# Kernel optimization log

Hardware: AMD Instinct MI355X
Metric: run time of the kernel (lower is better)

Reference implementation:

```python
import math
import jax, jax.numpy as jnp
import numpy as np

B, L, C, H = 8, 1024, 1024, 16
D = C // H  # head_dim = 64
MAX_SCALE_MUL = math.log(100.0)


def setup_inputs() -> dict:
    key = jax.random.key(0)
    ks = jax.random.split(key, 8)
    x = jax.random.normal(ks[0], (B, L, C), dtype=jnp.float32)
    # rotary frequencies: angle(l, j) = l * theta^(-2j/D), stored as (cos, sin)
    theta = 10000.0
    inv_freq = theta ** (-jnp.arange(0, D, 2, dtype=jnp.float32) / D)  # [D/2]
    ang = jnp.arange(L, dtype=jnp.float32)[:, None] * inv_freq[None, :]  # [L, D/2]
    freqs_cis = jnp.stack([jnp.cos(ang), jnp.sin(ang)], axis=-1)  # [L, D/2, 2]
    attn_bias = jnp.zeros((1, 1, L, L), dtype=jnp.float32)
    W_qkv = jax.random.normal(ks[1], (3 * C, C), dtype=jnp.float32) * (1.0 / math.sqrt(C))
    q_bias = jnp.zeros((C,), dtype=jnp.float32)
    v_bias = jnp.zeros((C,), dtype=jnp.float32)
    scale_mul_log = jnp.full((1, H, 1, 1), math.log(4.0), dtype=jnp.float32)
    W_proj = jax.random.normal(ks[2], (C, C), dtype=jnp.float32) * (1.0 / math.sqrt(C))
    b_proj = jnp.zeros((C,), dtype=jnp.float32)
    return {"x": x, "freqs_cis": freqs_cis, "attn_bias": attn_bias,
            "W_qkv": W_qkv, "q_bias": q_bias, "v_bias": v_bias,
            "scale_mul_log": scale_mul_log, "W_proj": W_proj, "b_proj": b_proj}


def _l2norm(t):
    # F.normalize(t, dim=-1): t / max(||t||_2, eps)
    n = jnp.sqrt(jnp.sum(t * t, axis=-1, keepdims=True))
    return t / jnp.maximum(n, 1e-12)


def _rope(t, fr):
    # t: [B,H,L,D]; fr: [L,D/2,2] (cos,sin). Complex mul on adjacent pairs.
    b, h, l, d = t.shape
    t2 = t.reshape(b, h, l, d // 2, 2)
    c = fr[None, None, :, :, 0]
    s = fr[None, None, :, :, 1]
    re = t2[..., 0] * c - t2[..., 1] * s
    im = t2[..., 0] * s + t2[..., 1] * c
    return jnp.stack([re, im], axis=-1).reshape(b, h, l, d)


def reference(x, freqs_cis, attn_bias, W_qkv, q_bias, v_bias, scale_mul_log, W_proj, b_proj):
    b, l, c = x.shape
    bias = jnp.concatenate([q_bias, jnp.zeros_like(q_bias), v_bias])  # [3C]
    qkv = (x @ W_qkv.T + bias).reshape(b, l, 3, H, D)
    # permute(2,0,3,1,4) -> q,k,v each [B,H,L,D]
    q = jnp.transpose(qkv[:, :, 0], (0, 2, 1, 3))
    k = jnp.transpose(qkv[:, :, 1], (0, 2, 1, 3))
    v = jnp.transpose(qkv[:, :, 2], (0, 2, 1, 3))
    # attn_l2_norm path: learned per-head scale, softmax scale = 1
    scale_mul = jnp.exp(jnp.minimum(scale_mul_log, MAX_SCALE_MUL))  # [1,H,1,1]
    q = _l2norm(q) * scale_mul
    k = _l2norm(k)
    q = _rope(q, freqs_cis)
    k = _rope(k, freqs_cis)
    scores = jnp.einsum('bhqd,bhkd->bhqk', q, k) * 1.0 + attn_bias
    attn = jax.nn.softmax(scores, axis=-1)
    out = jnp.einsum('bhqk,bhkd->bhqd', attn, v)
    out = jnp.transpose(out, (0, 2, 1, 3)).reshape(b, l, c)
    return out @ W_proj.T + b_proj
```

## Files before the change

kernel.cpp:

```cpp
#include <hip/hip_runtime.h>
#include <math.h>

#define PB 8
#define PL 1024
#define PC 1024
#define PH 16
#define PD 64
#define MAX_SCALE_MUL 4.605170185988092f
#define LOG2E 1.4426950408889634f

typedef __attribute__((ext_vector_type(8))) short s16x8;
typedef __attribute__((ext_vector_type(4))) float f32x4;

#define MFMA16(a, b, c) __builtin_amdgcn_mfma_f32_16x16x32_bf16(a, b, c, 0, 0, 0)

#if __has_builtin(__builtin_amdgcn_exp2f)
#define EXP2(x) __builtin_amdgcn_exp2f(x)
#else
#define EXP2(x) exp2f(x)
#endif

__device__ __forceinline__ unsigned short f2bf(float f) {
    unsigned u = __float_as_uint(f);
    unsigned r = (u + 0x7fffu + ((u >> 16) & 1u)) >> 16;
    return (unsigned short)r;
}

__device__ __forceinline__ unsigned pk2bf(float a, float b) {
#if __has_builtin(__builtin_amdgcn_cvt_pk_bf16_f32)
    typedef __attribute__((ext_vector_type(2))) __bf16 bf16x2_t;
    bf16x2_t r = __builtin_amdgcn_cvt_pk_bf16_f32(a, b);
    return __builtin_bit_cast(unsigned, r);
#else
    return (unsigned)f2bf(a) | ((unsigned)f2bf(b) << 16);
#endif
}

__device__ __forceinline__ void gl2lds16(const void* g, void* l) {
    __builtin_amdgcn_global_load_lds(
        (const __attribute__((address_space(1))) unsigned int*)g,
        (__attribute__((address_space(3))) unsigned int*)l, 16, 0, 0);
}

__global__ __launch_bounds__(256) void cast3f_kernel(
    const float* __restrict__ a, const float* __restrict__ b,
    const float* __restrict__ c, const float* __restrict__ bias,
    unsigned short* __restrict__ oa, unsigned short* __restrict__ ob,
    unsigned short* __restrict__ oc, int* __restrict__ flag)
{
    int blk = blockIdx.x;
    if (blk >= 12288) {
        int idx = (blk - 12288) * 256 + threadIdx.x;
        const float4* b4 = (const float4*)bias;
        bool nz = false;
#pragma unroll
        for (int i = 0; i < 4; i++) {
            float4 v = b4[idx * 4 + i];
            nz |= (v.x != 0.f) | (v.y != 0.f) | (v.z != 0.f) | (v.w != 0.f);
        }
        if (nz) atomicOr(flag, 1);
        return;
    }
    const float* src; unsigned short* dst; int base;
    if (blk < 8192)       { src = a; dst = oa; base = blk; }
    else if (blk < 11264) { src = b; dst = ob; base = blk - 8192; }
    else                  { src = c; dst = oc; base = blk - 11264; }
    int i = base * 256 + threadIdx.x;
    float4 v = ((const float4*)src)[i];
    ((uint2*)dst)[i] = make_uint2(pk2bf(v.x, v.y), pk2bf(v.z, v.w));
}

template<int VMODE>
__global__ __launch_bounds__(256) void gemm_qkv_lean(
    const unsigned short* __restrict__ Xh,
    const unsigned short* __restrict__ Wh,
    const float* __restrict__ qb, const float* __restrict__ vb,
    const float* __restrict__ freqs,
    unsigned short* __restrict__ Qh, unsigned short* __restrict__ Kh,
    unsigned short* __restrict__ Vt)
{
    __shared__ unsigned short As[128 * 64];
    __shared__ unsigned short Bs[128 * 64];
    const int tid  = threadIdx.x;
    const int wave = tid >> 6, lane = tid & 63;
    const int wm = wave & 1, wn = wave >> 1;
    const int quad = lane >> 4, rr = lane & 15;
    const int m0 = blockIdx.x * 128;
    const int n0 = (blockIdx.y + (VMODE ? 16 : 0)) * 128;

    f32x4 acc[4][4];
#pragma unroll
    for (int i = 0; i < 4; i++)
#pragma unroll
        for (int j = 0; j < 4; j++) acc[i][j] = (f32x4){0.f, 0.f, 0.f, 0.f};

    const int r8 = lane >> 3;
    const int c8 = lane & 7;
    const int g  = c8 ^ r8;
    const unsigned short* gA = Xh + (size_t)(m0 + wave * 32 + r8) * 1024 + g * 8;
    const unsigned short* gB = Wh + (size_t)(n0 + wave * 32 + r8) * 1024 + g * 8;
    unsigned short* lA = &As[(wave * 32) * 64];
    unsigned short* lB = &Bs[(wave * 32) * 64];

    const int swz8 = rr & 7;

    for (int k0 = 0; k0 < 16; k0++) {
#pragma unroll
        for (int t = 0; t < 4; t++) {
            gl2lds16(gA + (size_t)t * 8192, &lA[(t * 8) * 64]);
            gl2lds16(gB + (size_t)t * 8192, &lB[(t * 8) * 64]);
        }
        gA += 64; gB += 64;
        __syncthreads();

#pragma unroll
        for (int kk = 0; kk < 2; kk++) {
            const int coff = ((kk * 4 + quad) ^ swz8) * 8;
            s16x8 wf[4], xf[4];
#pragma unroll
            for (int i = 0; i < 4; i++)
                wf[i] = *(const s16x8*)&Bs[(wn * 64 + i * 16 + rr) * 64 + coff];
#pragma unroll
            for (int j = 0; j < 4; j++)
                xf[j] = *(const s16x8*)&As[(wm * 64 + j * 16 + rr) * 64 + coff];
            if constexpr (VMODE == 0) {
#pragma unroll
                for (int i = 0; i < 4; i++)
#pragma unroll
                    for (int j = 0; j < 4; j++)
                        acc[i][j] = MFMA16(wf[i], xf[j], acc[i][j]);
            } else {
#pragma unroll
                for (int i = 0; i < 4; i++)
#pragma unroll
                    for (int j = 0; j < 4; j++)
                        acc[i][j] = MFMA16(xf[j], wf[i], acc[i][j]);
            }
        }
        __syncthreads();
    }

    const int b   = m0 >> 10;
    const int h   = ((n0 & 1023) + wn * 64) >> 6;
    const int lb0 = (m0 & 1023) + wm * 64;

    if constexpr (VMODE) {
        unsigned short* basep = Vt + (size_t)(b * PH + h) * PD * PL;
#pragma unroll
        for (int i = 0; i < 4; i++) {
            const int d = i * 16 + rr;
            const float bv = vb[h * 64 + d];
#pragma unroll
            for (int j = 0; j < 4; j++) {
                const int l0 = lb0 + j * 16 + quad * 4;
                uint2 pk = make_uint2(pk2bf(acc[i][j][0] + bv, acc[i][j][1] + bv),
                                      pk2bf(acc[i][j][2] + bv, acc[i][j][3] + bv));
                *(uint2*)(basep + (size_t)d * PL + l0) = pk;
            }
        }
    } else {
        const int which = n0 >> 10;
        if (which == 0) {
            unsigned short* basep = Qh + (size_t)(b * PH + h) * PL * PD;
#pragma unroll
            for (int i = 0; i < 4; i++) {
                const int d0 = i * 16 + quad * 4;
                const float4 b4 = *(const float4*)(qb + h * 64 + d0);
#pragma unroll
                for (int j = 0; j < 4; j++) {
                    const int l = lb0 + j * 16 + rr;
                    uint2 pk = make_uint2(
                        pk2bf(acc[i][j][0] + b4.x, acc[i][j][1] + b4.y),
                        pk2bf(acc[i][j][2] + b4.z, acc[i][j][3] + b4.w));
                    *(uint2*)(basep + (size_t)l * PD + d0) = pk;
                }
            }
        } else {
            unsigned short* basep = Kh + (size_t)(b * PH + h) * PL * PD;
            const float2* fr2 = (const float2*)freqs;
#pragma unroll
            for (int j = 0; j < 4; j++) {
                float ss = 0.f;
#pragma unroll
                for (int i = 0; i < 4; i++)
                    ss = fmaf(acc[i][j][0], acc[i][j][0],
                         fmaf(acc[i][j][1], acc[i][j][1],
                         fmaf(acc[i][j][2], acc[i][j][2],
                         fmaf(acc[i][j][3], acc[i][j][3], ss))));
                ss += __shfl_xor(ss, 16);
                ss += __shfl_xor(ss, 32);
                const float scale = 1.0f / fmaxf(sqrtf(ss), 1e-12f);
                const int l = lb0 + j * 16 + rr;
#pragma unroll
                for (int i = 0; i < 4; i++) {
                    const int d0 = i * 16 + quad * 4;
                    const float2 cs0 = fr2[(size_t)l * 32 + (d0 >> 1)];
                    const float2 cs1 = fr2[(size_t)l * 32 + (d0 >> 1) + 1];
                    const float a0 = acc[i][j][0] * scale, a1 = acc[i][j][1] * scale;
                    const float a2 = acc[i][j][2] * scale, a3 = acc[i][j][3] * scale;
                    uint2 pk = make_uint2(
                        pk2bf(a0 * cs0.x - a1 * cs0.y, fmaf(a0, cs0.y, a1 * cs0.x)),
                        pk2bf(a2 * cs1.x - a3 * cs1.y, fmaf(a2, cs1.y, a3 * cs1.x)));
                    *(uint2*)(basep + (size_t)l * PD + d0) = pk;
                }
            }
        }
    }
}

__global__ __launch_bounds__(256) void attn_mfma(
    const unsigned short* __restrict__ Qh, const unsigned short* __restrict__ Kh,
    const unsigned short* __restrict__ Vt, const float* __restrict__ bias,
    const float* __restrict__ sml, const int* __restrict__ biasflag,
    const float* __restrict__ freqs, unsigned short* __restrict__ O)
{
    __shared__ unsigned short Ks[2][64 * 64];
    __shared__ unsigned short Vs[2][64 * 64];
    __shared__ unsigned int   Ps[4][16 * 32];

    const int tid  = threadIdx.x;
    const int wave = tid >> 6, lane = tid & 63;
    const int quad = lane >> 4, rr = lane & 15;
    const int bh = blockIdx.x, q0 = blockIdx.y * 128;
    const int b = bh >> 4, h = bh & 15;
    const int hasbias = *biasflag;

    const float M = __expf(fminf(sml[h], MAX_SCALE_MUL)) * LOG2E;
    const f32x4 negM = (f32x4){-M, -M, -M, -M};

    const int sr = wave * 16 + (lane >> 3);
    const int sc = lane & 7;
    const int sg = sc ^ (sr & 7);
    const int swz8 = rr & 7;
    const int psw  = (rr & 7) << 2;

    const size_t kvbase = (size_t)bh * PL * PD;
    const float2* fr2 = (const float2*)freqs;

    auto stage = [&](int buf, int kb) {
        gl2lds16(Kh + kvbase + (size_t)(kb * 64 + sr) * PD + sg * 8,
                 &Ks[buf][(wave * 16) * 64]);
        gl2lds16(Kh + kvbase + (size_t)(kb * 64 + sr + 8) * PD + sg * 8,
                 &Ks[buf][(wave * 16 + 8) * 64]);
        gl2lds16(Vt + kvbase + (size_t)sr * PL + kb * 64 + sg * 8,
                 &Vs[buf][(wave * 16) * 64]);
        gl2lds16(Vt + kvbase + (size_t)(sr + 8) * PL + kb * 64 + sg * 8,
                 &Vs[buf][(wave * 16 + 8) * 64]);
    };

    stage(0, 0);

    s16x8 qB[2][2];
#pragma unroll
    for (int g = 0; g < 2; g++) {
        const int ql = q0 + g * 64 + wave * 16 + rr;
        const size_t qoff = ((size_t)bh * PL + ql) * PD;
        uint4 r0 = *(const uint4*)(Qh + qoff + quad * 8);
        uint4 r1 = *(const uint4*)(Qh + qoff + 32 + quad * 8);
        unsigned uu[8] = {r0.x, r0.y, r0.z, r0.w, r1.x, r1.y, r1.z, r1.w};
        float lo[8], hi[8];
        float ss = 0.f;
#pragma unroll
        for (int m = 0; m < 8; m++) {
            lo[m] = __uint_as_float(uu[m] << 16);
            hi[m] = __uint_as_float(uu[m] & 0xffff0000u);
            ss = fmaf(lo[m], lo[m], fmaf(hi[m], hi[m], ss));
        }
        ss += __shfl_xor(ss, 16);
        ss += __shfl_xor(ss, 32);
        const float scale = M / fmaxf(sqrtf(ss), 1e-12f);
        unsigned outw[8];
#pragma unroll
        for (int m = 0; m < 8; m++) {
            const int idx = (m >> 2) * 16 + quad * 4 + (m & 3);
            float2 cs = fr2[(size_t)ql * 32 + idx];
            float av = lo[m] * scale, bv = hi[m] * scale;
            float re = av * cs.x - bv * cs.y;
            float im = fmaf(av, cs.y, bv * cs.x);
            outw[m] = pk2bf(re, im);
        }
        uint4 w0 = make_uint4(outw[0], outw[1], outw[2], outw[3]);
        uint4 w1 = make_uint4(outw[4], outw[5], outw[6], outw[7]);
        qB[g][0] = __builtin_bit_cast(s16x8, w0);
        qB[g][1] = __builtin_bit_cast(s16x8, w1);
    }

    f32x4 accO[2][4];
#pragma unroll
    for (int g = 0; g < 2; g++)
#pragma unroll
        for (int jd = 0; jd < 4; jd++) accO[g][jd] = (f32x4){0.f, 0.f, 0.f, 0.f};
    float lsum[2] = {0.f, 0.f};

    __syncthreads();

    int cur = 0;
    for (int kb = 0; kb < 16; kb++) {
        if (kb < 15) stage(cur ^ 1, kb + 1);

        s16x8 kA[4][2];
#pragma unroll
        for (int s = 0; s < 4; s++) {
            kA[s][0] = *(const s16x8*)&Ks[cur][(s * 16 + rr) * 64 + ((0 + quad) ^ swz8) * 8];
            kA[s][1] = *(const s16x8*)&Ks[cur][(s * 16 + rr) * 64 + ((4 + quad) ^ swz8) * 8];
        }
        f32x4 sc4[2][4];
        __builtin_amdgcn_s_setprio(1);
#pragma unroll
        for (int g = 0; g < 2; g++)
#pragma unroll
            for (int s = 0; s < 4; s++) {
                f32x4 z = MFMA16(kA[s][0], qB[g][0], negM);
                z = MFMA16(kA[s][1], qB[g][1], z);
                sc4[g][s] = z;
            }
        __builtin_amdgcn_s_setprio(0);

        if (hasbias) {
#pragma unroll
            for (int g = 0; g < 2; g++) {
                const float* brow = bias + (size_t)(q0 + g * 64 + wave * 16 + rr) * PL + kb * 64;
#pragma unroll
                for (int s = 0; s < 4; s++) {
                    float4 bv = *(const float4*)(brow + s * 16 + quad * 4);
                    sc4[g][s][0] = fmaf(bv.x, LOG2E, sc4[g][s][0]);
                    sc4[g][s][1] = fmaf(bv.y, LOG2E, sc4[g][s][1]);
                    sc4[g][s][2] = fmaf(bv.z, LOG2E, sc4[g][s][2]);
                    sc4[g][s][3] = fmaf(bv.w, LOG2E, sc4[g][s][3]);
                }
            }
        }

#pragma unroll
        for (int g = 0; g < 2; g++) {
#pragma unroll
            for (int s = 0; s < 4; s++) {
                sc4[g][s][0] = EXP2(sc4[g][s][0]);
                sc4[g][s][1] = EXP2(sc4[g][s][1]);
                sc4[g][s][2] = EXP2(sc4[g][s][2]);
                sc4[g][s][3] = EXP2(sc4[g][s][3]);
            }
            f32x4 ls4 = (sc4[g][0] + sc4[g][1]) + (sc4[g][2] + sc4[g][3]);
            lsum[g] += (ls4[0] + ls4[1]) + (ls4[2] + ls4[3]);
        }

        s16x8 vA[4][2];
#pragma unroll
        for (int s = 0; s < 4; s++) {
            vA[s][0] = *(const s16x8*)&Vs[cur][(s * 16 + rr) * 64 + ((0 + quad) ^ swz8) * 8];
            vA[s][1] = *(const s16x8*)&Vs[cur][(s * 16 + rr) * 64 + ((4 + quad) ^ swz8) * 8];
        }
#pragma unroll
        for (int g = 0; g < 2; g++) {
#pragma unroll
            for (int s = 0; s < 4; s++) {
                *(uint2*)&Ps[wave][rr * 32 + ((s * 8 + quad * 2) ^ psw)] =
                    make_uint2(pk2bf(sc4[g][s][0], sc4[g][s][1]),
                               pk2bf(sc4[g][s][2], sc4[g][s][3]));
            }
            s16x8 pB0 = *(const s16x8*)&Ps[wave][rr * 32 + ((quad * 4) ^ psw)];
            s16x8 pB1 = *(const s16x8*)&Ps[wave][rr * 32 + ((16 + quad * 4) ^ psw)];
            __builtin_amdgcn_s_setprio(1);
#pragma unroll
            for (int jd = 0; jd < 4; jd++) {
                accO[g][jd] = MFMA16(vA[jd][0], pB0, accO[g][jd]);
                accO[g][jd] = MFMA16(vA[jd][1], pB1, accO[g][jd]);
            }
            __builtin_amdgcn_s_setprio(0);
        }

        __syncthreads();
        cur ^= 1;
    }

    const int lr = lane >> 2, cch = lane & 3;
    const int pswl = (lr & 7) << 2;
#pragma unroll
    for (int g = 0; g < 2; g++) {
        float ls = lsum[g];
        ls += __shfl_xor(ls, 16);
        ls += __shfl_xor(ls, 32);
        float inv = 1.0f / ls;
#pragma unroll
        for (int jd = 0; jd < 4; jd++) {
            *(uint2*)&Ps[wave][rr * 32 + ((jd * 8 + quad * 2) ^ psw)] =
                make_uint2(pk2bf(accO[g][jd][0] * inv, accO[g][jd][1] * inv),
                           pk2bf(accO[g][jd][2] * inv, accO[g][jd][3] * inv));
        }
        uint4 w0 = *(const uint4*)&Ps[wave][lr * 32 + ((cch * 8) ^ pswl)];
        uint4 w1 = *(const uint4*)&Ps[wave][lr * 32 + ((cch * 8 + 4) ^ pswl)];
        size_t ob = ((size_t)(b * PL + q0 + g * 64 + wave * 16 + lr) * PC + h * PD);
        *(uint4*)(O + ob + cch * 16)     = w0;
        *(uint4*)(O + ob + cch * 16 + 8) = w1;
    }
}

__global__ __launch_bounds__(256) void gemm_proj_mfma(
    const unsigned short* __restrict__ Ah,
    const unsigned short* __restrict__ Wh,
    const float* __restrict__ bp, float* __restrict__ Out)
{
    __shared__ unsigned short As[128 * 64];
    __shared__ unsigned short Bs[128 * 64];
    const int tid  = threadIdx.x;
    const int wave = tid >> 6, lane = tid & 63;
    const int wm = wave & 1, wn = wave >> 1;
    const int quad = lane >> 4, rr = lane & 15;
    const int m0 = blockIdx.x * 128, n0 = blockIdx.y * 128;

    f32x4 acc[4][4];
#pragma unroll
    for (int i = 0; i < 4; i++)
#pragma unroll
        for (int j = 0; j < 4; j++) acc[i][j] = (f32x4){0.f, 0.f, 0.f, 0.f};

    const int r8 = lane >> 3;
    const int c8 = lane & 7;
    const int g  = c8 ^ r8;
    const unsigned short* gA = Ah + (size_t)(m0 + wave * 32 + r8) * 1024 + g * 8;
    const unsigned short* gB = Wh + (size_t)(n0 + wave * 32 + r8) * 1024 + g * 8;
    unsigned short* lA = &As[(wave * 32) * 64];
    unsigned short* lB = &Bs[(wave * 32) * 64];

    const int swz8 = rr & 7;

    for (int k0 = 0; k0 < 16; k0++) {
#pragma unroll
        for (int t = 0; t < 4; t++) {
            gl2lds16(gA + (size_t)t * 8192, &lA[(t * 8) * 64]);
            gl2lds16(gB + (size_t)t * 8192, &lB[(t * 8) * 64]);
        }
        gA += 64; gB += 64;
        __syncthreads();

#pragma unroll
        for (int kk = 0; kk < 2; kk++) {
            const int coff = ((kk * 4 + quad) ^ swz8) * 8;
            s16x8 wf[4], xf[4];
#pragma unroll
            for (int i = 0; i < 4; i++)
                wf[i] = *(const s16x8*)&Bs[(wn * 64 + i * 16 + rr) * 64 + coff];
#pragma unroll
            for (int j = 0; j < 4; j++)
                xf[j] = *(const s16x8*)&As[(wm * 64 + j * 16 + rr) * 64 + coff];
#pragma unroll
            for (int i = 0; i < 4; i++)
#pragma unroll
                for (int j = 0; j < 4; j++)
                    acc[i][j] = MFMA16(wf[i], xf[j], acc[i][j]);
        }
        __syncthreads();
    }

#pragma unroll
    for (int i = 0; i < 4; i++) {
        const int nn = n0 + wn * 64 + i * 16 + quad * 4;
        const float4 bb = *(const float4*)(bp + nn);
#pragma unroll
        for (int j = 0; j < 4; j++) {
            const int m = m0 + wm * 64 + j * 16 + rr;
            float4 o = make_float4(acc[i][j][0] + bb.x, acc[i][j][1] + bb.y,
                                   acc[i][j][2] + bb.z, acc[i][j][3] + bb.w);
            *(float4*)(Out + (size_t)m * 1024 + nn) = o;
        }
    }
}

extern "C" void kernel_launch(void* const* d_in, const int* in_sizes, int n_in,
                              void* d_out, int out_size, void* d_ws, size_t ws_size,
                              hipStream_t stream)
{
    const float* x         = (const float*)d_in[0];
    const float* freqs     = (const float*)d_in[1];
    const float* attn_bias = (const float*)d_in[2];
    const float* W_qkv     = (const float*)d_in[3];
    const float* q_bias    = (const float*)d_in[4];
    const float* v_bias    = (const float*)d_in[5];
    const float* sml       = (const float*)d_in[6];
    const float* W_proj    = (const float*)d_in[7];
    const float* b_proj    = (const float*)d_in[8];
    float* out = (float*)d_out;

    unsigned char* w = (unsigned char*)d_ws;
    const size_t MB = 1ull << 20;
    unsigned short* xh  = (unsigned short*)(w + 0);
    unsigned short* wqh = (unsigned short*)(w + 16 * MB);
    unsigned short* wph = (unsigned short*)(w + 22 * MB);
    unsigned short* Qh  = (unsigned short*)(w + 24 * MB);
    unsigned short* Kh  = (unsigned short*)(w + 40 * MB);
    unsigned short* Vt  = (unsigned short*)(w + 72 * MB);
    unsigned short* Oh  = (unsigned short*)(w + 88 * MB);
    int*            flg = (int*)(w + 104 * MB);

    hipMemsetAsync(flg, 0, sizeof(int), stream);
    cast3f_kernel<<<12544, 256, 0, stream>>>(x, W_qkv, W_proj, attn_bias,
                                             xh, wqh, wph, flg);
    gemm_qkv_lean<0><<<dim3(64, 16), 256, 0, stream>>>(
        xh, wqh, q_bias, v_bias, freqs, Qh, Kh, Vt);
    gemm_qkv_lean<1><<<dim3(64, 8), 256, 0, stream>>>(
        xh, wqh, q_bias, v_bias, freqs, Qh, Kh, Vt);
    attn_mfma<<<dim3(128, 8), 256, 0, stream>>>(Qh, Kh, Vt, attn_bias, sml, flg, freqs, Oh);
    gemm_proj_mfma<<<dim3(64, 8), 256, 0, stream>>>(Oh, wph, b_proj, out);
}
```

Baseline: 266.3 us.

## Restructure attention inner loop to cut register pressure and target three blocks per CU

```diff
diff --git a/kernel.cpp b/kernel.cpp
--- a/kernel.cpp
+++ b/kernel.cpp
@@ -208,7 +208,7 @@
     }
 }
 
-__global__ __launch_bounds__(256) void attn_mfma(
+__global__ __launch_bounds__(256, 3) void attn_mfma(
     const unsigned short* __restrict__ Qh, const unsigned short* __restrict__ Kh,
     const unsigned short* __restrict__ Vt, const float* __restrict__ bias,
     const float* __restrict__ sml, const int* __restrict__ biasflag,
@@ -298,73 +298,52 @@
     for (int kb = 0; kb < 16; kb++) {
         if (kb < 15) stage(cur ^ 1, kb + 1);
 
-        s16x8 kA[4][2];
+        unsigned ps[2][4][2];
 #pragma unroll
         for (int s = 0; s < 4; s++) {
-            kA[s][0] = *(const s16x8*)&Ks[cur][(s * 16 + rr) * 64 + ((0 + quad) ^ swz8) * 8];
-            kA[s][1] = *(const s16x8*)&Ks[cur][(s * 16 + rr) * 64 + ((4 + quad) ^ swz8) * 8];
-        }
-        f32x4 sc4[2][4];
-        __builtin_amdgcn_s_setprio(1);
-#pragma unroll
-        for (int g = 0; g < 2; g++)
-#pragma unroll
-            for (int s = 0; s < 4; s++) {
-                f32x4 z = MFMA16(kA[s][0], qB[g][0], negM);
-                z = MFMA16(kA[s][1], qB[g][1], z);
-                sc4[g][s] = z;
-            }
-        __builtin_amdgcn_s_setprio(0);
-
-        if (hasbias) {
+            const s16x8 k0 = *(const s16x8*)&Ks[cur][(s * 16 + rr) * 64 + ((0 + quad) ^ swz8) * 8];
+            const s16x8 k1 = *(const s16x8*)&Ks[cur][(s * 16 + rr) * 64 + ((4 + quad) ^ swz8) * 8];
 #pragma unroll
             for (int g = 0; g < 2; g++) {
-                const float* brow = bias + (size_t)(q0 + g * 64 + wave * 16 + rr) * PL + kb * 64;
-#pragma unroll
-                for (int s = 0; s < 4; s++) {
+                __builtin_amdgcn_s_setprio(1);
+                f32x4 z = MFMA16(k0, qB[g][0], negM);
+                z = MFMA16(k1, qB[g][1], z);
+                __builtin_amdgcn_s_setprio(0);
+                if (hasbias) {
+                    const float* brow = bias + (size_t)(q0 + g * 64 + wave * 16 + rr) * PL + kb * 64;
                     float4 bv = *(const float4*)(brow + s * 16 + quad * 4);
-                    sc4[g][s][0] = fmaf(bv.x, LOG2E, sc4[g][s][0]);
-                    sc4[g][s][1] = fmaf(bv.y, LOG2E, sc4[g][s][1]);
-                    sc4[g][s][2] = fmaf(bv.z, LOG2E, sc4[g][s][2]);
-                    sc4[g][s][3] = fmaf(bv.w, LOG2E, sc4[g][s][3]);
+                    z[0] = fmaf(bv.x, LOG2E, z[0]);
+                    z[1] = fmaf(bv.y, LOG2E, z[1]);
+                    z[2] = fmaf(bv.z, LOG2E, z[2]);
+                    z[3] = fmaf(bv.w, LOG2E, z[3]);
                 }
-            }
-        }
-
+                z[0] = EXP2(z[0]); z[1] = EXP2(z[1]);
+                z[2] = EXP2(z[2]); z[3] = EXP2(z[3]);
+                lsum[g] += (z[0] + z[1]) + (z[2] + z[3]);
+                ps[g][s][0] = pk2bf(z[0], z[1]);
+                ps[g][s][1] = pk2bf(z[2], z[3]);
+            }
+        }
+
+        s16x8 pB[2][2];
 #pragma unroll
         for (int g = 0; g < 2; g++) {
 #pragma unroll
-            for (int s = 0; s < 4; s++) {
-                sc4[g][s][0] = EXP2(sc4[g][s][0]);
-                sc4[g][s][1] = EXP2(sc4[g][s][1]);
-                sc4[g][s][2] = EXP2(sc4[g][s][2]);
-                sc4[g][s][3] = EXP2(sc4[g][s][3]);
-            }
-            f32x4 ls4 = (sc4[g][0] + sc4[g][1]) + (sc4[g][2] + sc4[g][3]);
-            lsum[g] += (ls4[0] + ls4[1]) + (ls4[2] + ls4[3]);
-        }
-
-        s16x8 vA[4][2];
-#pragma unroll
-        for (int s = 0; s < 4; s++) {
-            vA[s][0] = *(const s16x8*)&Vs[cur][(s * 16 + rr) * 64 + ((0 + quad) ^ swz8) * 8];
-            vA[s][1] = *(const s16x8*)&Vs[cur][(s * 16 + rr) * 64 + ((4 + quad) ^ swz8) * 8];
-        }
-#pragma unroll
-        for (int g = 0; g < 2; g++) {
-#pragma unroll
-            for (int s = 0; s < 4; s++) {
+            for (int s = 0; s < 4; s++)
                 *(uint2*)&Ps[wave][rr * 32 + ((s * 8 + quad * 2) ^ psw)] =
-                    make_uint2(pk2bf(sc4[g][s][0], sc4[g][s][1]),
-                               pk2bf(sc4[g][s][2], sc4[g][s][3]));
-            }
-            s16x8 pB0 = *(const s16x8*)&Ps[wave][rr * 32 + ((quad * 4) ^ psw)];
-            s16x8 pB1 = *(const s16x8*)&Ps[wave][rr * 32 + ((16 + quad * 4) ^ psw)];
+                    make_uint2(ps[g][s][0], ps[g][s][1]);
+            pB[g][0] = *(const s16x8*)&Ps[wave][rr * 32 + ((quad * 4) ^ psw)];
+            pB[g][1] = *(const s16x8*)&Ps[wave][rr * 32 + ((16 + quad * 4) ^ psw)];
+        }
+#pragma unroll
+        for (int jd = 0; jd < 4; jd++) {
+            const s16x8 v0 = *(const s16x8*)&Vs[cur][(jd * 16 + rr) * 64 + ((0 + quad) ^ swz8) * 8];
+            const s16x8 v1 = *(const s16x8*)&Vs[cur][(jd * 16 + rr) * 64 + ((4 + quad) ^ swz8) * 8];
             __builtin_amdgcn_s_setprio(1);
 #pragma unroll
-            for (int jd = 0; jd < 4; jd++) {
-                accO[g][jd] = MFMA16(vA[jd][0], pB0, accO[g][jd]);
-                accO[g][jd] = MFMA16(vA[jd][1], pB1, accO[g][jd]);
+            for (int g = 0; g < 2; g++) {
+                accO[g][jd] = MFMA16(v0, pB[g][0], accO[g][jd]);
+                accO[g][jd] = MFMA16(v1, pB[g][1], accO[g][jd]);
             }
             __builtin_amdgcn_s_setprio(0);
         }
```

Measured after the change: 268.5 us. No clear change (+0.8%).
